# Kernel tuning notes

Hardware: AMD Instinct MI355X
Metric: run time of the kernel (lower is better)

Reference implementation:

```python
import jax, jax.numpy as jnp
import numpy as np

B, S, D, H = 2, 2048, 1024, 16
HD = D // H
LN_EPS = 1e-5


def setup_inputs() -> dict:
    key = jax.random.key(0)
    ks = jax.random.split(key, 8)
    inv = 1.0 / np.sqrt(D)
    return {
        "embedded": jax.random.normal(ks[0], (B, S, D), dtype=jnp.float32),
        "Wq": jax.random.normal(ks[1], (D, D), dtype=jnp.float32) * inv,
        "bq": jax.random.normal(ks[2], (D,), dtype=jnp.float32) * 0.01,
        "Wk": jax.random.normal(ks[3], (D, D), dtype=jnp.float32) * inv,
        "bk": jax.random.normal(ks[4], (D,), dtype=jnp.float32) * 0.01,
        "Wv": jax.random.normal(ks[5], (D, D), dtype=jnp.float32) * inv,
        "bv": jax.random.normal(ks[6], (D,), dtype=jnp.float32) * 0.01,
        "gamma": jnp.ones((D,), dtype=jnp.float32),
        "beta": jnp.zeros((D,), dtype=jnp.float32),
    }


def reference(embedded, Wq, bq, Wk, bk, Wv, bv, gamma, beta):
    b, s, d = embedded.shape
    # QKV projections (torch Linear: x @ W^T + b)
    q = embedded @ Wq.T + bq
    k = embedded @ Wk.T + bk
    v = embedded @ Wv.T + bv
    # [b, s, H, hd] -> [b, H, s, hd]
    q = q.reshape(b, s, H, HD).transpose(0, 2, 1, 3)
    k = k.reshape(b, s, H, HD).transpose(0, 2, 1, 3)
    v = v.reshape(b, s, H, HD).transpose(0, 2, 1, 3)
    # scores [b, H, s, s]
    qk = jnp.einsum("bhqd,bhkd->bhqk", q, k)
    # NaN scrub -> -inf (original: qk[qk != qk] = -inf)
    qk = jnp.where(jnp.isnan(qk), -jnp.inf, qk)
    # NOTE: original scales by sqrt(shape[-1]) == sqrt(seq_len), not head_dim
    qk = qk / jnp.float32(np.sqrt(s))
    p = jax.nn.softmax(qk, axis=-1)
    p = jnp.where(jnp.isnan(p), 0.0, p)
    v = jnp.where(jnp.isnan(v), 0.0, v)
    # post-softmax upper-triangular (incl. diagonal) mask, no renormalization
    mask = jnp.triu(jnp.ones((s, s), dtype=p.dtype), k=0)
    p = p * mask
    z = jnp.einsum("bhqk,bhkd->bhqd", p, v)  # [b, H, s, hd]
    # original does a raw .view(b, s, -1) on contiguous [b,h,s,hd] (no transpose)
    z = z.reshape(b, s, d)
    # residual + LayerNorm
    x = embedded + z
    mu = jnp.mean(x, axis=-1, keepdims=True)
    var = jnp.mean(jnp.square(x - mu), axis=-1, keepdims=True)
    out = (x - mu) * jax.lax.rsqrt(var + LN_EPS) * gamma + beta
    return out
```

## Files before the change

kernel.cpp:

```cpp
#include <hip/hip_runtime.h>
#include <hip/hip_bf16.h>
#include <math.h>

typedef unsigned short ushort_t;
typedef unsigned char uchar_t;
typedef __attribute__((ext_vector_type(8))) short short8;
typedef __attribute__((ext_vector_type(4))) float f32x4;

struct __align__(8) us4 { ushort_t u[4]; };

__device__ __forceinline__ ushort_t f2bf(float x) {
  union { float f; unsigned u; } c; c.f = x;
  unsigned r = c.u + 0x7FFFu + ((c.u >> 16) & 1u);
  return (ushort_t)(r >> 16);
}
__device__ __forceinline__ float bf2f(ushort_t b) {
  union { unsigned u; float f; } c; c.u = ((unsigned)b) << 16;
  return c.f;
}

__global__ __launch_bounds__(256) void cvt_kernel(const float* __restrict__ src,
                                                  ushort_t* __restrict__ dst, int n) {
  int i = (blockIdx.x * 256 + threadIdx.x) * 4;
  if (i < n) {
    f32x4 v = *(const f32x4*)(src + i);
    us4 o;
    o.u[0] = f2bf(v[0]); o.u[1] = f2bf(v[1]); o.u[2] = f2bf(v[2]); o.u[3] = f2bf(v[3]);
    *(us4*)(dst + i) = o;
  }
}

struct QkvArgs {
  const ushort_t* X;
  const ushort_t* W0; const ushort_t* W1; const ushort_t* W2;
  const float* b0; const float* b1; const float* b2;
  ushort_t* o0; ushort_t* o1; ushort_t* o2;
};

__global__ __launch_bounds__(256) void qkv_gemm(QkvArgs a) {
  __shared__ __align__(16) ushort_t As[128 * 32];
  __shared__ __align__(16) ushort_t Bs[128 * 32];
  const int z = blockIdx.z;
  const ushort_t* W  = (z == 0) ? a.W0 : ((z == 1) ? a.W1 : a.W2);
  const float* bias  = (z == 0) ? a.b0 : ((z == 1) ? a.b1 : a.b2);
  ushort_t* out      = (z == 0) ? a.o0 : ((z == 1) ? a.o1 : a.o2);
  const int swz = (z == 1) ? 7 : 0;
  const int mBase = blockIdx.x * 128;
  const int nBase = blockIdx.y * 128;
  const int tid  = threadIdx.x;
  const int lane = tid & 63;
  const int w    = tid >> 6;
  const int wm   = w >> 1, wn = w & 1;
  const int quad = lane >> 4;
  const int l15  = lane & 15;

  f32x4 acc[4][4] = {};

  const int srow = lane >> 2;
  const int scol = (lane & 3) * 8;
  const ushort_t* gA0 = a.X + (mBase + srow) * 1024 + scol;
  const ushort_t* gB0 = W   + (nBase + srow) * 1024 + scol;

  for (int k0 = 0; k0 < 1024; k0 += 32) {
#pragma unroll
    for (int p = 0; p < 2; ++p) {
      int rr = (w * 2 + p) * 16;
      __builtin_amdgcn_global_load_lds(
          (const __attribute__((address_space(1))) void*)(gA0 + rr * 1024 + k0),
          (__attribute__((address_space(3))) void*)(As + (w * 2 + p) * 512), 16, 0, 0);
      __builtin_amdgcn_global_load_lds(
          (const __attribute__((address_space(1))) void*)(gB0 + rr * 1024 + k0),
          (__attribute__((address_space(3))) void*)(Bs + (w * 2 + p) * 512), 16, 0, 0);
    }
    __syncthreads();
    short8 af[4], bfr[4];
#pragma unroll
    for (int mi = 0; mi < 4; ++mi)
      af[mi] = *(const short8*)(As + (wm * 64 + mi * 16 + l15) * 32 + quad * 8);
#pragma unroll
    for (int ni = 0; ni < 4; ++ni)
      bfr[ni] = *(const short8*)(Bs + (wn * 64 + ni * 16 + l15) * 32 + quad * 8);
#pragma unroll
    for (int mi = 0; mi < 4; ++mi)
#pragma unroll
      for (int ni = 0; ni < 4; ++ni)
        acc[mi][ni] = __builtin_amdgcn_mfma_f32_16x16x32_bf16(af[mi], bfr[ni], acc[mi][ni], 0, 0, 0);
    __syncthreads();
  }

#pragma unroll
  for (int ni = 0; ni < 4; ++ni) {
    int n = nBase + wn * 64 + ni * 16 + l15;
    float bv = bias[n];
    int h = n >> 6, hd = n & 63;
    int hdHi = hd >> 3, hdLo = hd & 7;
#pragma unroll
    for (int mi = 0; mi < 4; ++mi) {
      int m0 = mBase + wm * 64 + mi * 16 + quad * 4;
#pragma unroll
      for (int r = 0; r < 4; ++r) {
        int m = m0 + r;
        int bb = m >> 11, s = m & 2047;
        int hdw = (((hdHi ^ (s & swz)) << 3) | hdLo);
        out[((bb * 16 + h) * 2048 + s) * 64 + hdw] = f2bf(acc[mi][ni][r] + bv);
      }
    }
  }
}

__global__ __launch_bounds__(256) void tr_kernel(const ushort_t* __restrict__ vb,
                                                 uchar_t* __restrict__ vT) {
  __shared__ uchar_t Ls[64 * 68];
  int bh = blockIdx.y;
  int s0 = blockIdx.x * 64;
  int tid = threadIdx.x;
  const ushort_t* vp = vb + (size_t)bh * 131072;
  uchar_t* op = vT + (size_t)bh * 131072;
#pragma unroll
  for (int p = 0; p < 2; ++p) {
    int c = p * 256 + tid;
    int row = c >> 3, u = c & 7;
    short8 x = *(const short8*)(vp + (size_t)(s0 + row) * 64 + u * 8);
    float f0 = bf2f((ushort_t)x[0]), f1 = bf2f((ushort_t)x[1]);
    float f2 = bf2f((ushort_t)x[2]), f3 = bf2f((ushort_t)x[3]);
    float f4 = bf2f((ushort_t)x[4]), f5 = bf2f((ushort_t)x[5]);
    float f6 = bf2f((ushort_t)x[6]), f7 = bf2f((ushort_t)x[7]);
    unsigned int lo = __builtin_amdgcn_cvt_pk_fp8_f32(f0, f1, 0, false);
    lo = __builtin_amdgcn_cvt_pk_fp8_f32(f2, f3, lo, true);
    unsigned int hi = __builtin_amdgcn_cvt_pk_fp8_f32(f4, f5, 0, false);
    hi = __builtin_amdgcn_cvt_pk_fp8_f32(f6, f7, hi, true);
    *(unsigned int*)(Ls + row * 68 + u * 8)     = lo;
    *(unsigned int*)(Ls + row * 68 + u * 8 + 4) = hi;
  }
  __syncthreads();
#pragma unroll
  for (int p = 0; p < 4; ++p) {
    int oc = p * 256 + tid;
    int hd = oc >> 4, sc = oc & 15;
    unsigned int v = 0;
#pragma unroll
    for (int i = 0; i < 4; ++i)
      v |= ((unsigned int)Ls[(sc * 4 + i) * 68 + hd]) << (8 * i);
    int u = ((s0 & 64) >> 4) + (sc >> 2);
    int dest = (s0 & ~127) + ((u ^ (hd & 7)) * 16) + (sc & 3) * 4;
    *(unsigned int*)(op + (size_t)hd * 2048 + dest) = v;
  }
}

__global__ __launch_bounds__(256) void attn_kernel(const ushort_t* __restrict__ qb,
                                                   const ushort_t* __restrict__ kb,
                                                   const uchar_t* __restrict__ vT,
                                                   ushort_t* __restrict__ zb) {
  __shared__ __align__(16) ushort_t Ks[128 * 64];
  __shared__ __align__(16) uchar_t  Vt[64 * 128];
  __shared__ __align__(16) uchar_t  Ps[128 * 128];
  const int bh   = blockIdx.y;
  const int qblk = blockIdx.x * 128;
  const int tid  = threadIdx.x;
  const int lane = tid & 63;
  const int w    = tid >> 6;
  const int quad = lane >> 4;
  const int l15  = lane & 15;
  const int l7   = l15 & 7;
  const float cexp = 0.02209708691f * 1.44269504089f;

  const ushort_t* qpage = qb + (size_t)bh * (2048 * 64);
  const ushort_t* kpage = kb + (size_t)bh * (2048 * 64);
  const uchar_t*  vpage = vT + (size_t)bh * (64 * 2048);

  short8 qf[2][2];
#pragma unroll
  for (int nb = 0; nb < 2; ++nb) {
    int qg = qblk + w * 32 + nb * 16 + l15;
#pragma unroll
    for (int kd = 0; kd < 2; ++kd)
      qf[nb][kd] = *(const short8*)(qpage + (size_t)qg * 64 + kd * 32 + quad * 8);
  }

  float psum[2] = {0.f, 0.f};
  f32x4 o[4][2] = {};

  for (int kt = 0; kt < 2048; kt += 128) {
    const bool needV = (kt + 127 >= qblk);
    const bool needP = (kt + 127 >= qblk + w * 32);
    __syncthreads();

#pragma unroll
    for (int p = 0; p < 4; ++p) {
      int j = w * 4 + p;
      __builtin_amdgcn_global_load_lds(
          (const __attribute__((address_space(1))) void*)(kpage + (size_t)kt * 64 + j * 512 + lane * 8),
          (__attribute__((address_space(3))) void*)(Ks + j * 512), 16, 0, 0);
    }
    if (needV) {
#pragma unroll
      for (int p = 0; p < 2; ++p) {
        int j = w * 2 + p;
        __builtin_amdgcn_global_load_lds(
            (const __attribute__((address_space(1))) void*)(vpage + (size_t)(j * 8 + (lane >> 3)) * 2048 + kt + (lane & 7) * 16),
            (__attribute__((address_space(3))) void*)(Vt + j * 1024), 16, 0, 0);
      }
    }
    __syncthreads();

#pragma unroll
    for (int mb = 0; mb < 8; ++mb) {
      const ushort_t* krow = Ks + (mb * 16 + l15) * 64;
      short8 kf0 = *(const short8*)(krow + ((0 + quad) ^ l7) * 8);
      short8 kf1 = *(const short8*)(krow + ((4 + quad) ^ l7) * 8);
      f32x4 s0 = {}, s1 = {};
      s0 = __builtin_amdgcn_mfma_f32_16x16x32_bf16(kf0, qf[0][0], s0, 0, 0, 0);
      s0 = __builtin_amdgcn_mfma_f32_16x16x32_bf16(kf1, qf[0][1], s0, 0, 0, 0);
      s1 = __builtin_amdgcn_mfma_f32_16x16x32_bf16(kf0, qf[1][0], s1, 0, 0, 0);
      s1 = __builtin_amdgcn_mfma_f32_16x16x32_bf16(kf1, qf[1][1], s1, 0, 0, 0);
      const int keyb = kt + mb * 16 + quad * 4;
#pragma unroll
      for (int nb = 0; nb < 2; ++nb) {
        f32x4 s = nb ? s1 : s0;
        float p0 = __builtin_amdgcn_exp2f(s[0] * cexp);
        float p1 = __builtin_amdgcn_exp2f(s[1] * cexp);
        float p2 = __builtin_amdgcn_exp2f(s[2] * cexp);
        float p3 = __builtin_amdgcn_exp2f(s[3] * cexp);
        psum[nb] += (p0 + p1) + (p2 + p3);
        if (needP) {
          int qg = qblk + w * 32 + nb * 16 + l15;
          float m0 = (keyb + 0 >= qg) ? p0 : 0.f;
          float m1 = (keyb + 1 >= qg) ? p1 : 0.f;
          float m2 = (keyb + 2 >= qg) ? p2 : 0.f;
          float m3 = (keyb + 3 >= qg) ? p3 : 0.f;
          unsigned int pk = __builtin_amdgcn_cvt_pk_fp8_f32(m0, m1, 0, false);
          pk = __builtin_amdgcn_cvt_pk_fp8_f32(m2, m3, pk, true);
          *(unsigned int*)(Ps + (w * 32 + nb * 16 + l15) * 128 + ((mb ^ l7) * 16) + quad * 4) = pk;
        }
      }
    }

    if (needP) {
#pragma unroll
      for (int kd = 0; kd < 4; ++kd) {
        const int un = ((kd * 2 + (quad >> 1)) ^ l7) * 16 + (quad & 1) * 8;
        long long pf0 = *(const long long*)(Ps + (w * 32 + l15) * 128 + un);
        long long pf1 = *(const long long*)(Ps + (w * 32 + 16 + l15) * 128 + un);
#pragma unroll
        for (int mb = 0; mb < 4; ++mb) {
          long long vf = *(const long long*)(Vt + (mb * 16 + l15) * 128 + un);
          o[mb][0] = __builtin_amdgcn_mfma_f32_16x16x32_fp8_fp8(vf, pf0, o[mb][0], 0, 0, 0);
          o[mb][1] = __builtin_amdgcn_mfma_f32_16x16x32_fp8_fp8(vf, pf1, o[mb][1], 0, 0, 0);
        }
      }
    }
  }

#pragma unroll
  for (int nb = 0; nb < 2; ++nb) {
    psum[nb] += __shfl_xor(psum[nb], 16, 64);
    psum[nb] += __shfl_xor(psum[nb], 32, 64);
    float rl = 1.0f / psum[nb];
    int qg = qblk + w * 32 + nb * 16 + l15;
#pragma unroll
    for (int mb = 0; mb < 4; ++mb)
#pragma unroll
      for (int r = 0; r < 4; ++r) {
        int hd = mb * 16 + quad * 4 + r;
        zb[((size_t)bh * 2048 + qg) * 64 + hd] = f2bf(o[mb][nb][r] * rl);
      }
  }
}

__global__ __launch_bounds__(256) void ln_kernel(const float* __restrict__ emb,
                                                 const ushort_t* __restrict__ zb,
                                                 const float* __restrict__ gamma,
                                                 const float* __restrict__ beta,
                                                 float* __restrict__ out) {
  __shared__ float red[2][4];
  int row = blockIdx.x;
  int b = row >> 11, s = row & 2047;
  int h = s >> 7;
  int siHi = (s & 127) << 4;
  int tid = threadIdx.x;
  int dcol = tid * 4;
  int si = siHi | (dcol >> 6);
  int j = dcol & 63;

  f32x4 e4 = *(const f32x4*)(emb + (size_t)row * 1024 + dcol);
  us4 z4 = *(const us4*)(zb + (((size_t)(b * 16 + h) * 2048 + si) * 64 + j));
  float x0 = e4[0] + bf2f(z4.u[0]);
  float x1 = e4[1] + bf2f(z4.u[1]);
  float x2 = e4[2] + bf2f(z4.u[2]);
  float x3 = e4[3] + bf2f(z4.u[3]);

  float sum = x0 + x1 + x2 + x3;
  float sq  = x0 * x0 + x1 * x1 + x2 * x2 + x3 * x3;
#pragma unroll
  for (int off = 1; off <= 32; off <<= 1) {
    sum += __shfl_xor(sum, off, 64);
    sq  += __shfl_xor(sq,  off, 64);
  }
  int wv = tid >> 6;
  if ((tid & 63) == 0) { red[0][wv] = sum; red[1][wv] = sq; }
  __syncthreads();
  float ts = red[0][0] + red[0][1] + red[0][2] + red[0][3];
  float tq = red[1][0] + red[1][1] + red[1][2] + red[1][3];
  float mu = ts * (1.0f / 1024.0f);
  float var = tq * (1.0f / 1024.0f) - mu * mu;
  float rsig = rsqrtf(var + 1e-5f);

  f32x4 g4 = *(const f32x4*)(gamma + dcol);
  f32x4 b4 = *(const f32x4*)(beta + dcol);
  f32x4 o4;
  o4[0] = (x0 - mu) * rsig * g4[0] + b4[0];
  o4[1] = (x1 - mu) * rsig * g4[1] + b4[1];
  o4[2] = (x2 - mu) * rsig * g4[2] + b4[2];
  o4[3] = (x3 - mu) * rsig * g4[3] + b4[3];
  *(f32x4*)(out + (size_t)row * 1024 + dcol) = o4;
}

extern "C" void kernel_launch(void* const* d_in, const int* in_sizes, int n_in,
                              void* d_out, int out_size, void* d_ws, size_t ws_size,
                              hipStream_t stream) {
  (void)in_sizes; (void)n_in; (void)out_size; (void)ws_size;
  const float* emb   = (const float*)d_in[0];
  const float* Wq    = (const float*)d_in[1];
  const float* bq    = (const float*)d_in[2];
  const float* Wk    = (const float*)d_in[3];
  const float* bk    = (const float*)d_in[4];
  const float* Wv    = (const float*)d_in[5];
  const float* bv    = (const float*)d_in[6];
  const float* gamma = (const float*)d_in[7];
  const float* beta  = (const float*)d_in[8];
  float* out = (float*)d_out;

  char* ws = (char*)d_ws;
  ushort_t* Xbf  = (ushort_t*)(ws);
  ushort_t* Wqb  = (ushort_t*)(ws + 8388608);
  ushort_t* Wkb  = (ushort_t*)(ws + 10485760);
  ushort_t* Wvb  = (ushort_t*)(ws + 12582912);
  ushort_t* qbuf = (ushort_t*)(ws + 14680064);
  ushort_t* kbuf = (ushort_t*)(ws + 23068672);
  ushort_t* vbuf = (ushort_t*)(ws + 31457280);
  ushort_t* zbuf = (ushort_t*)(ws + 31457280);
  uchar_t*  vTb  = (uchar_t*)(ws + 39845888);

  cvt_kernel<<<4096, 256, 0, stream>>>(emb, Xbf, 4194304);
  cvt_kernel<<<1024, 256, 0, stream>>>(Wq, Wqb, 1048576);
  cvt_kernel<<<1024, 256, 0, stream>>>(Wk, Wkb, 1048576);
  cvt_kernel<<<1024, 256, 0, stream>>>(Wv, Wvb, 1048576);

  QkvArgs a;
  a.X = Xbf;
  a.W0 = Wqb; a.W1 = Wkb; a.W2 = Wvb;
  a.b0 = bq;  a.b1 = bk;  a.b2 = bv;
  a.o0 = qbuf; a.o1 = kbuf; a.o2 = vbuf;
  qkv_gemm<<<dim3(32, 8, 3), 256, 0, stream>>>(a);

  tr_kernel<<<dim3(32, 32), 256, 0, stream>>>(vbuf, vTb);

  attn_kernel<<<dim3(16, 32), 256, 0, stream>>>(qbuf, kbuf, vTb, zbuf);

  ln_kernel<<<4096, 256, 0, stream>>>(emb, zbuf, gamma, beta, out);
}
```

Baseline: 197.0 us.

## Fuse V transpose into QKV epilogue, merge conversions, add MFMA priority hints

After: 201.7 us. 1.02x slower.

```diff
diff --git a/kernel.cpp b/kernel.cpp
--- a/kernel.cpp
+++ b/kernel.cpp
@@ -19,22 +19,26 @@
   return c.f;
 }
 
-__global__ __launch_bounds__(256) void cvt_kernel(const float* __restrict__ src,
-                                                  ushort_t* __restrict__ dst, int n) {
-  int i = (blockIdx.x * 256 + threadIdx.x) * 4;
-  if (i < n) {
-    f32x4 v = *(const f32x4*)(src + i);
-    us4 o;
-    o.u[0] = f2bf(v[0]); o.u[1] = f2bf(v[1]); o.u[2] = f2bf(v[2]); o.u[3] = f2bf(v[3]);
-    *(us4*)(dst + i) = o;
-  }
+struct CvtArgs { const float* s[4]; ushort_t* d[4]; };
+
+__global__ __launch_bounds__(256) void cvt_all(CvtArgs c) {
+  int bid = blockIdx.x;
+  int job, base;
+  if (bid < 4096) { job = 0; base = bid; }
+  else { job = 1 + ((bid - 4096) >> 10); base = (bid - 4096) & 1023; }
+  int i = (base * 256 + threadIdx.x) * 4;
+  f32x4 v = *(const f32x4*)(c.s[job] + i);
+  us4 o;
+  o.u[0] = f2bf(v[0]); o.u[1] = f2bf(v[1]); o.u[2] = f2bf(v[2]); o.u[3] = f2bf(v[3]);
+  *(us4*)(c.d[job] + i) = o;
 }
 
 struct QkvArgs {
   const ushort_t* X;
   const ushort_t* W0; const ushort_t* W1; const ushort_t* W2;
   const float* b0; const float* b1; const float* b2;
-  ushort_t* o0; ushort_t* o1; ushort_t* o2;
+  ushort_t* o0; ushort_t* o1;
+  uchar_t* vt;
 };
 
 __global__ __launch_bounds__(256) void qkv_gemm(QkvArgs a) {
@@ -43,8 +47,6 @@
   const int z = blockIdx.z;
   const ushort_t* W  = (z == 0) ? a.W0 : ((z == 1) ? a.W1 : a.W2);
   const float* bias  = (z == 0) ? a.b0 : ((z == 1) ? a.b1 : a.b2);
-  ushort_t* out      = (z == 0) ? a.o0 : ((z == 1) ? a.o1 : a.o2);
-  const int swz = (z == 1) ? 7 : 0;
   const int mBase = blockIdx.x * 128;
   const int nBase = blockIdx.y * 128;
   const int tid  = threadIdx.x;
@@ -88,62 +90,45 @@
     __syncthreads();
   }
 
-#pragma unroll
-  for (int ni = 0; ni < 4; ++ni) {
-    int n = nBase + wn * 64 + ni * 16 + l15;
-    float bv = bias[n];
-    int h = n >> 6, hd = n & 63;
-    int hdHi = hd >> 3, hdLo = hd & 7;
-#pragma unroll
-    for (int mi = 0; mi < 4; ++mi) {
-      int m0 = mBase + wm * 64 + mi * 16 + quad * 4;
-#pragma unroll
-      for (int r = 0; r < 4; ++r) {
-        int m = m0 + r;
-        int bb = m >> 11, s = m & 2047;
-        int hdw = (((hdHi ^ (s & swz)) << 3) | hdLo);
-        out[((bb * 16 + h) * 2048 + s) * 64 + hdw] = f2bf(acc[mi][ni][r] + bv);
-      }
-    }
-  }
-}
-
-__global__ __launch_bounds__(256) void tr_kernel(const ushort_t* __restrict__ vb,
-                                                 uchar_t* __restrict__ vT) {
-  __shared__ uchar_t Ls[64 * 68];
-  int bh = blockIdx.y;
-  int s0 = blockIdx.x * 64;
-  int tid = threadIdx.x;
-  const ushort_t* vp = vb + (size_t)bh * 131072;
-  uchar_t* op = vT + (size_t)bh * 131072;
-#pragma unroll
-  for (int p = 0; p < 2; ++p) {
-    int c = p * 256 + tid;
-    int row = c >> 3, u = c & 7;
-    short8 x = *(const short8*)(vp + (size_t)(s0 + row) * 64 + u * 8);
-    float f0 = bf2f((ushort_t)x[0]), f1 = bf2f((ushort_t)x[1]);
-    float f2 = bf2f((ushort_t)x[2]), f3 = bf2f((ushort_t)x[3]);
-    float f4 = bf2f((ushort_t)x[4]), f5 = bf2f((ushort_t)x[5]);
-    float f6 = bf2f((ushort_t)x[6]), f7 = bf2f((ushort_t)x[7]);
-    unsigned int lo = __builtin_amdgcn_cvt_pk_fp8_f32(f0, f1, 0, false);
-    lo = __builtin_amdgcn_cvt_pk_fp8_f32(f2, f3, lo, true);
-    unsigned int hi = __builtin_amdgcn_cvt_pk_fp8_f32(f4, f5, 0, false);
-    hi = __builtin_amdgcn_cvt_pk_fp8_f32(f6, f7, hi, true);
-    *(unsigned int*)(Ls + row * 68 + u * 8)     = lo;
-    *(unsigned int*)(Ls + row * 68 + u * 8 + 4) = hi;
-  }
-  __syncthreads();
-#pragma unroll
-  for (int p = 0; p < 4; ++p) {
-    int oc = p * 256 + tid;
-    int hd = oc >> 4, sc = oc & 15;
-    unsigned int v = 0;
-#pragma unroll
-    for (int i = 0; i < 4; ++i)
-      v |= ((unsigned int)Ls[(sc * 4 + i) * 68 + hd]) << (8 * i);
-    int u = ((s0 & 64) >> 4) + (sc >> 2);
-    int dest = (s0 & ~127) + ((u ^ (hd & 7)) * 16) + (sc & 3) * 4;
-    *(unsigned int*)(op + (size_t)hd * 2048 + dest) = v;
+  if (z == 2) {
+#pragma unroll
+    for (int ni = 0; ni < 4; ++ni) {
+      int n = nBase + wn * 64 + ni * 16 + l15;
+      float bv = bias[n];
+      int h = n >> 6, hd = n & 63;
+#pragma unroll
+      for (int mi = 0; mi < 4; ++mi) {
+        int m0 = mBase + wm * 64 + mi * 16 + quad * 4;
+        int bb = m0 >> 11, s = m0 & 2047;
+        float x0 = acc[mi][ni][0] + bv, x1 = acc[mi][ni][1] + bv;
+        float x2 = acc[mi][ni][2] + bv, x3 = acc[mi][ni][3] + bv;
+        unsigned int pk = __builtin_amdgcn_cvt_pk_fp8_f32(x0, x1, 0, false);
+        pk = __builtin_amdgcn_cvt_pk_fp8_f32(x2, x3, pk, true);
+        int dest = (s & ~127) + ((((s >> 4) & 7) ^ (hd & 7)) * 16) + (s & 15);
+        *(unsigned int*)(a.vt + (size_t)(bb * 16 + h) * 131072 + (size_t)hd * 2048 + dest) = pk;
+      }
+    }
+  } else {
+    ushort_t* out = (z == 0) ? a.o0 : a.o1;
+    const int swz = (z == 1) ? 7 : 0;
+#pragma unroll
+    for (int ni = 0; ni < 4; ++ni) {
+      int n = nBase + wn * 64 + ni * 16 + l15;
+      float bv = bias[n];
+      int h = n >> 6, hd = n & 63;
+      int hdHi = hd >> 3, hdLo = hd & 7;
+#pragma unroll
+      for (int mi = 0; mi < 4; ++mi) {
+        int m0 = mBase + wm * 64 + mi * 16 + quad * 4;
+#pragma unroll
+        for (int r = 0; r < 4; ++r) {
+          int m = m0 + r;
+          int bb = m >> 11, s = m & 2047;
+          int hdw = (((hdHi ^ (s & swz)) << 3) | hdLo);
+          out[((bb * 16 + h) * 2048 + s) * 64 + hdw] = f2bf(acc[mi][ni][r] + bv);
+        }
+      }
+    }
   }
 }
 
@@ -209,10 +194,12 @@
       short8 kf0 = *(const short8*)(krow + ((0 + quad) ^ l7) * 8);
       short8 kf1 = *(const short8*)(krow + ((4 + quad) ^ l7) * 8);
       f32x4 s0 = {}, s1 = {};
+      __builtin_amdgcn_s_setprio(1);
       s0 = __builtin_amdgcn_mfma_f32_16x16x32_bf16(kf0, qf[0][0], s0, 0, 0, 0);
       s0 = __builtin_amdgcn_mfma_f32_16x16x32_bf16(kf1, qf[0][1], s0, 0, 0, 0);
       s1 = __builtin_amdgcn_mfma_f32_16x16x32_bf16(kf0, qf[1][0], s1, 0, 0, 0);
       s1 = __builtin_amdgcn_mfma_f32_16x16x32_bf16(kf1, qf[1][1], s1, 0, 0, 0);
+      __builtin_amdgcn_s_setprio(0);
       const int keyb = kt + mb * 16 + quad * 4;
 #pragma unroll
       for (int nb = 0; nb < 2; ++nb) {
@@ -241,12 +228,14 @@
         const int un = ((kd * 2 + (quad >> 1)) ^ l7) * 16 + (quad & 1) * 8;
         long long pf0 = *(const long long*)(Ps + (w * 32 + l15) * 128 + un);
         long long pf1 = *(const long long*)(Ps + (w * 32 + 16 + l15) * 128 + un);
+        __builtin_amdgcn_s_setprio(1);
 #pragma unroll
         for (int mb = 0; mb < 4; ++mb) {
           long long vf = *(const long long*)(Vt + (mb * 16 + l15) * 128 + un);
           o[mb][0] = __builtin_amdgcn_mfma_f32_16x16x32_fp8_fp8(vf, pf0, o[mb][0], 0, 0, 0);
           o[mb][1] = __builtin_amdgcn_mfma_f32_16x16x32_fp8_fp8(vf, pf1, o[mb][1], 0, 0, 0);
         }
+        __builtin_amdgcn_s_setprio(0);
       }
     }
   }
@@ -337,24 +326,22 @@
   ushort_t* Wvb  = (ushort_t*)(ws + 12582912);
   ushort_t* qbuf = (ushort_t*)(ws + 14680064);
   ushort_t* kbuf = (ushort_t*)(ws + 23068672);
-  ushort_t* vbuf = (ushort_t*)(ws + 31457280);
   ushort_t* zbuf = (ushort_t*)(ws + 31457280);
   uchar_t*  vTb  = (uchar_t*)(ws + 39845888);
 
-  cvt_kernel<<<4096, 256, 0, stream>>>(emb, Xbf, 4194304);
-  cvt_kernel<<<1024, 256, 0, stream>>>(Wq, Wqb, 1048576);
-  cvt_kernel<<<1024, 256, 0, stream>>>(Wk, Wkb, 1048576);
-  cvt_kernel<<<1024, 256, 0, stream>>>(Wv, Wvb, 1048576);
+  CvtArgs c;
+  c.s[0] = emb; c.s[1] = Wq; c.s[2] = Wk; c.s[3] = Wv;
+  c.d[0] = Xbf; c.d[1] = Wqb; c.d[2] = Wkb; c.d[3] = Wvb;
+  cvt_all<<<7168, 256, 0, stream>>>(c);
 
   QkvArgs a;
   a.X = Xbf;
   a.W0 = Wqb; a.W1 = Wkb; a.W2 = Wvb;
   a.b0 = bq;  a.b1 = bk;  a.b2 = bv;
-  a.o0 = qbuf; a.o1 = kbuf; a.o2 = vbuf;
+  a.o0 = qbuf; a.o1 = kbuf;
+  a.vt = vTb;
   qkv_gemm<<<dim3(32, 8, 3), 256, 0, stream>>>(a);
 
-  tr_kernel<<<dim3(32, 32), 256, 0, stream>>>(vbuf, vTb);
-
   attn_kernel<<<dim3(16, 32), 256, 0, stream>>>(qbuf, kbuf, vTb, zbuf);
 
   ln_kernel<<<4096, 256, 0, stream>>>(emb, zbuf, gamma, beta, out);
```
